# Kernel tuning notes

Hardware: AMD Instinct MI355X
Metric: run time of the kernel (lower is better)

## Reference

```python
import jax, jax.numpy as jnp
import numpy as np

N = 10000          # nodes
E = 160000         # edges (avg degree 16)
F = 240            # invariant features_dim
H_INV, D_INV = 4, 60    # invariant heads / head dim
H_EV, D_EV = 3, 80      # equivariant heads (= len(degrees)) / head dim
RBF = 32
DEGREES = [1, 2, 3]
REPEATS = np.array([2 * l + 1 for l in DEGREES])   # [3,5,7]
EV_DIM = int(REPEATS.sum())                        # 15
OFFS = np.concatenate([[0], np.cumsum(REPEATS)])   # [0,3,8,15]


def _kaiming_uniform(key, shape, fan_in):
    # torch kaiming_uniform_ with a=sqrt(5): bound = 1/sqrt(fan_in)
    b = 1.0 / np.sqrt(fan_in)
    return jax.random.uniform(key, shape, minval=-b, maxval=b, dtype=jnp.float32)


def setup_inputs() -> dict:
    key = jax.random.key(0)
    ks = jax.random.split(key, 16)
    return {
        "inv_features": jax.random.normal(ks[0], (N, F), dtype=jnp.float32),
        "ev_features": jax.random.normal(ks[1], (N, EV_DIM), dtype=jnp.float32),
        "rbf": jax.random.uniform(ks[2], (E, RBF), dtype=jnp.float32),
        "sh_vectors": jax.random.normal(ks[3], (E, EV_DIM), dtype=jnp.float32),
        "cutoffs": jax.random.uniform(ks[4], (E, 1), dtype=jnp.float32),
        "W_q_inv": _kaiming_uniform(ks[5], (H_INV, D_INV, D_INV), D_INV),
        "W_k_inv": _kaiming_uniform(ks[6], (H_INV, D_INV, D_INV), D_INV),
        "W_v_inv": _kaiming_uniform(ks[7], (H_INV, D_INV, D_INV), D_INV),
        "W_q_ev": _kaiming_uniform(ks[8], (H_EV, D_EV, D_EV), D_EV),
        "W_k_ev": _kaiming_uniform(ks[9], (H_EV, D_EV, D_EV), D_EV),
        "W_filt_inv": _kaiming_uniform(ks[10], (RBF + len(DEGREES), F), RBF + len(DEGREES)),
        "b_filt_inv": jnp.zeros((F,), dtype=jnp.float32),
        "W_filt_ev": _kaiming_uniform(ks[11], (RBF + len(DEGREES), F), RBF + len(DEGREES)),
        "b_filt_ev": jnp.zeros((F,), dtype=jnp.float32),
        "senders": jax.random.randint(ks[12], (E,), 0, N, dtype=jnp.int32),
        "receivers": jax.random.randint(ks[13], (E,), 0, N, dtype=jnp.int32),
    }


def reference(inv_features, ev_features, rbf, sh_vectors, cutoffs,
              W_q_inv, W_k_inv, W_v_inv, W_q_ev, W_k_ev,
              W_filt_inv, b_filt_inv, W_filt_ev, b_filt_ev,
              senders, receivers):
    n = inv_features.shape[0]
    # edge-wise equivariant differences [E, 15]
    ev_diff = ev_features[senders] - ev_features[receivers]
    # per-degree SO3 invariants: sum over m components of each degree -> [E, 3]
    invs = jnp.stack([(ev_diff[:, OFFS[i]:OFFS[i + 1]] ** 2).sum(-1)
                      for i in range(len(DEGREES))], axis=-1)
    f_in = jnp.concatenate([rbf, invs], axis=-1)           # [E, RBF+3]
    fw_inv = (f_in @ W_filt_inv + b_filt_inv).reshape(-1, H_INV, D_INV)
    fw_ev = (f_in @ W_filt_ev + b_filt_ev).reshape(-1, H_EV, D_EV)

    xi = inv_features.reshape(-1, H_INV, D_INV)
    xe = inv_features.reshape(-1, H_EV, D_EV)
    q_inv = jnp.einsum('hij,nhi->nhj', W_q_inv, xi)[receivers]
    k_inv = jnp.einsum('hij,nhi->nhj', W_k_inv, xi)[senders]
    v_inv = jnp.einsum('hij,nhi->nhj', W_v_inv, xi)[senders]
    q_ev = jnp.einsum('hij,nhi->nhj', W_q_ev, xe)[receivers]
    k_ev = jnp.einsum('hij,nhi->nhj', W_k_ev, xe)[senders]

    alpha_inv = (q_inv * (k_inv * fw_inv)).sum(-1, keepdims=True) / np.sqrt(D_INV)  # [E,H,1]
    alpha_ev = (q_ev * (k_ev * fw_ev)).sum(-1) / np.sqrt(D_EV)                      # [E,3]

    scaled_inv = cutoffs[:, None] * alpha_inv * v_inv       # [E,H,D]
    d_inv = jax.ops.segment_sum(scaled_inv, receivers, num_segments=n).reshape(n, -1)

    alpha_ev_r = jnp.repeat(alpha_ev, REPEATS, axis=-1, total_repeat_length=EV_DIM)  # [E,15]
    scaled_ev = cutoffs * alpha_ev_r * sh_vectors
    d_ev = jax.ops.segment_sum(scaled_ev, receivers, num_segments=n)
    return d_inv, d_ev
```

## Files before the change

kernel.cpp:

```cpp
#include <hip/hip_runtime.h>

#define PNPB 16
#define ABLK 128
#define EPT  4

__global__ __launch_bounds__(256) void proj_kernel(
    const float* __restrict__ x,
    const float* __restrict__ Wq, const float* __restrict__ Wk,
    const float* __restrict__ Wv,
    const float* __restrict__ Wqe, const float* __restrict__ Wke,
    float* __restrict__ q_inv, float* __restrict__ k_inv,
    float* __restrict__ v_inv,
    float* __restrict__ q_ev, float* __restrict__ k_ev, int N)
{
    __shared__ float xs[PNPB * 240];
    const int base_node = blockIdx.x * PNPB;
    for (int idx = threadIdx.x; idx < PNPB * 240; idx += 256) {
        int g = base_node * 240 + idx;
        xs[idx] = (g < N * 240) ? x[g] : 0.f;
    }
    __syncthreads();

    const int slot = threadIdx.x & 63;
    const int wg   = threadIdx.x >> 6;
    if (slot >= 60) return;

    const int hi  = slot / 15;
    const int jdi = slot * 4 - hi * 60;
    const int he  = slot / 20;
    const int jde = slot * 4 - he * 80;
    const int nl0 = wg * 4;

    float4 aq[4], ak[4], av[4], aqe[4], ake[4];
    #pragma unroll
    for (int n = 0; n < 4; ++n) {
        aq[n] = make_float4(0.f,0.f,0.f,0.f); ak[n] = aq[n]; av[n] = aq[n];
        aqe[n] = aq[n]; ake[n] = aq[n];
    }
    {
        const float* wq = Wq + hi * 3600 + jdi;
        const float* wk = Wk + hi * 3600 + jdi;
        const float* wv = Wv + hi * 3600 + jdi;
        const float* xb = &xs[nl0 * 240 + hi * 60];
        #pragma unroll 2
        for (int i = 0; i < 60; ++i) {
            float xv0 = xb[i], xv1 = xb[240 + i], xv2 = xb[480 + i], xv3 = xb[720 + i];
            float4 w;
            w = *(const float4*)&wq[i * 60];
            aq[0].x += xv0*w.x; aq[0].y += xv0*w.y; aq[0].z += xv0*w.z; aq[0].w += xv0*w.w;
            aq[1].x += xv1*w.x; aq[1].y += xv1*w.y; aq[1].z += xv1*w.z; aq[1].w += xv1*w.w;
            aq[2].x += xv2*w.x; aq[2].y += xv2*w.y; aq[2].z += xv2*w.z; aq[2].w += xv2*w.w;
            aq[3].x += xv3*w.x; aq[3].y += xv3*w.y; aq[3].z += xv3*w.z; aq[3].w += xv3*w.w;
            w = *(const float4*)&wk[i * 60];
            ak[0].x += xv0*w.x; ak[0].y += xv0*w.y; ak[0].z += xv0*w.z; ak[0].w += xv0*w.w;
            ak[1].x += xv1*w.x; ak[1].y += xv1*w.y; ak[1].z += xv1*w.z; ak[1].w += xv1*w.w;
            ak[2].x += xv2*w.x; ak[2].y += xv2*w.y; ak[2].z += xv2*w.z; ak[2].w += xv2*w.w;
            ak[3].x += xv3*w.x; ak[3].y += xv3*w.y; ak[3].z += xv3*w.z; ak[3].w += xv3*w.w;
            w = *(const float4*)&wv[i * 60];
            av[0].x += xv0*w.x; av[0].y += xv0*w.y; av[0].z += xv0*w.z; av[0].w += xv0*w.w;
            av[1].x += xv1*w.x; av[1].y += xv1*w.y; av[1].z += xv1*w.z; av[1].w += xv1*w.w;
            av[2].x += xv2*w.x; av[2].y += xv2*w.y; av[2].z += xv2*w.z; av[2].w += xv2*w.w;
            av[3].x += xv3*w.x; av[3].y += xv3*w.y; av[3].z += xv3*w.z; av[3].w += xv3*w.w;
        }
    }
    {
        const float* wq = Wqe + he * 6400 + jde;
        const float* wk = Wke + he * 6400 + jde;
        const float* xb = &xs[nl0 * 240 + he * 80];
        #pragma unroll 2
        for (int i = 0; i < 80; ++i) {
            float xv0 = xb[i], xv1 = xb[240 + i], xv2 = xb[480 + i], xv3 = xb[720 + i];
            float4 w;
            w = *(const float4*)&wq[i * 80];
            aqe[0].x += xv0*w.x; aqe[0].y += xv0*w.y; aqe[0].z += xv0*w.z; aqe[0].w += xv0*w.w;
            aqe[1].x += xv1*w.x; aqe[1].y += xv1*w.y; aqe[1].z += xv1*w.z; aqe[1].w += xv1*w.w;
            aqe[2].x += xv2*w.x; aqe[2].y += xv2*w.y; aqe[2].z += xv2*w.z; aqe[2].w += xv2*w.w;
            aqe[3].x += xv3*w.x; aqe[3].y += xv3*w.y; aqe[3].z += xv3*w.z; aqe[3].w += xv3*w.w;
            w = *(const float4*)&wk[i * 80];
            ake[0].x += xv0*w.x; ake[0].y += xv0*w.y; ake[0].z += xv0*w.z; ake[0].w += xv0*w.w;
            ake[1].x += xv1*w.x; ake[1].y += xv1*w.y; ake[1].z += xv1*w.z; ake[1].w += xv1*w.w;
            ake[2].x += xv2*w.x; ake[2].y += xv2*w.y; ake[2].z += xv2*w.z; ake[2].w += xv2*w.w;
            ake[3].x += xv3*w.x; ake[3].y += xv3*w.y; ake[3].z += xv3*w.z; ake[3].w += xv3*w.w;
        }
    }
    #pragma unroll
    for (int n = 0; n < 4; ++n) {
        const int node = base_node + nl0 + n;
        if (node >= N) break;
        const int ob = node * 240 + slot * 4;
        *(float4*)&q_inv[ob] = aq[n];
        *(float4*)&k_inv[ob] = ak[n];
        *(float4*)&v_inv[ob] = av[n];
        *(float4*)&q_ev[ob]  = aqe[n];
        *(float4*)&k_ev[ob]  = ake[n];
    }
}

__global__ __launch_bounds__(256) void hist_kernel(
    const int* __restrict__ rcv, int* __restrict__ counts, int E)
{
    int e = blockIdx.x * 256 + threadIdx.x;
    if (e < E) atomicAdd(&counts[rcv[e]], 1);
}

__global__ __launch_bounds__(1024) void scan_kernel(
    const int* __restrict__ counts, int* __restrict__ rowstart,
    int* __restrict__ cursor, int N)
{
    __shared__ int wsum[16];
    __shared__ int carry_s;
    if (threadIdx.x == 0) carry_s = 0;
    __syncthreads();
    const int lane = threadIdx.x & 63;
    const int w    = threadIdx.x >> 6;
    for (int base = 0; base < N; base += 1024) {
        const int i = base + threadIdx.x;
        int v = (i < N) ? counts[i] : 0;
        int x = v;
        #pragma unroll
        for (int off = 1; off < 64; off <<= 1) {
            int t = __shfl_up(x, off);
            if (lane >= off) x += t;
        }
        if (lane == 63) wsum[w] = x;
        __syncthreads();
        if (w == 0) {
            int s = (lane < 16) ? wsum[lane] : 0;
            #pragma unroll
            for (int off = 1; off < 16; off <<= 1) {
                int t = __shfl_up(s, off);
                if (lane >= off) s += t;
            }
            if (lane < 16) wsum[lane] = s;
        }
        __syncthreads();
        const int woff = (w == 0) ? 0 : wsum[w - 1];
        const int ex = carry_s + woff + x - v;
        if (i < N) { rowstart[i] = ex; cursor[i] = ex; }
        __syncthreads();
        if (threadIdx.x == 1023) carry_s += wsum[15];
    }
    __syncthreads();
    if (threadIdx.x == 0) rowstart[N] = carry_s;
}

__global__ __launch_bounds__(256) void scatter_kernel(
    const int* __restrict__ rcv, int* __restrict__ cursor,
    int* __restrict__ csr, int E)
{
    int e = blockIdx.x * 256 + threadIdx.x;
    if (e < E) {
        int pos = atomicAdd(&cursor[rcv[e]], 1);
        csr[pos] = e;
    }
}

__global__ __launch_bounds__(ABLK, 2) void alpha_kernel(
    const float* __restrict__ ev_f, const float* __restrict__ rbf,
    const float* __restrict__ cut,
    const float* __restrict__ Wfi,  const float* __restrict__ bfi,
    const float* __restrict__ Wfe,  const float* __restrict__ bfe,
    const int* __restrict__ snd,    const int* __restrict__ rcv,
    const int* __restrict__ csr,
    const float* __restrict__ q_inv, const float* __restrict__ k_inv,
    const float* __restrict__ q_ev,  const float* __restrict__ k_ev,
    float* __restrict__ alpha, int E)
{
    __shared__ float WI[35 * 240];
    __shared__ float WE[35 * 240];
    __shared__ float BI[240];
    __shared__ float BE[240];
    for (int idx = threadIdx.x; idx < 35 * 240; idx += ABLK) {
        WI[idx] = Wfi[idx];
        WE[idx] = Wfe[idx];
    }
    for (int idx = threadIdx.x; idx < 240; idx += ABLK) {
        BI[idx] = bfi[idx];
        BE[idx] = bfe[idx];
    }
    __syncthreads();

    const float s60 = 0.12909944487358056f;
    const float s80 = 0.11180339887498948f;

    const int base = blockIdx.x * (ABLK * EPT);

    int ii[EPT], sN[EPT], rN[EPT];
    float cc[EPT];
    float f[EPT][35];
    #pragma unroll
    for (int t = 0; t < EPT; ++t) {
        int i = base + t * ABLK + threadIdx.x;
        if (i >= E) i = E - 1;
        ii[t] = i;
        const int e = csr[i];
        sN[t] = snd[e]; rN[t] = rcv[e]; cc[t] = cut[e];
        const float4* rb = (const float4*)(rbf + (size_t)e * 32);
        #pragma unroll
        for (int k4 = 0; k4 < 8; ++k4) {
            float4 v = rb[k4];
            f[t][k4*4+0] = v.x; f[t][k4*4+1] = v.y;
            f[t][k4*4+2] = v.z; f[t][k4*4+3] = v.w;
        }
        const float* es = ev_f + (size_t)sN[t] * 15;
        const float* er = ev_f + (size_t)rN[t] * 15;
        float i0 = 0.f, i1 = 0.f, i2 = 0.f;
        #pragma unroll
        for (int q = 0; q < 3; ++q)  { float d = es[q] - er[q]; i0 += d * d; }
        #pragma unroll
        for (int q = 3; q < 8; ++q)  { float d = es[q] - er[q]; i1 += d * d; }
        #pragma unroll
        for (int q = 8; q < 15; ++q) { float d = es[q] - er[q]; i2 += d * d; }
        f[t][32] = i0; f[t][33] = i1; f[t][34] = i2;
    }

    float out[EPT][8];

    #pragma unroll
    for (int h = 0; h < 4; ++h) {
        float acc[EPT];
        #pragma unroll
        for (int t = 0; t < EPT; ++t) acc[t] = 0.f;
        #pragma unroll 1
        for (int j4 = 0; j4 < 15; ++j4) {
            const int j = h * 60 + j4 * 4;
            const float4 b4 = *(const float4*)&BI[j];
            float4 fw[EPT];
            #pragma unroll
            for (int t = 0; t < EPT; ++t) fw[t] = b4;
            #pragma unroll
            for (int k = 0; k < 35; ++k) {
                const float4 w = *(const float4*)&WI[k * 240 + j];
                #pragma unroll
                for (int t = 0; t < EPT; ++t) {
                    const float fv = f[t][k];
                    fw[t].x += fv * w.x; fw[t].y += fv * w.y;
                    fw[t].z += fv * w.z; fw[t].w += fv * w.w;
                }
            }
            #pragma unroll
            for (int t = 0; t < EPT; ++t) {
                const float4 q  = *(const float4*)(q_inv + (size_t)rN[t] * 240 + j);
                const float4 kk = *(const float4*)(k_inv + (size_t)sN[t] * 240 + j);
                acc[t] += q.x * kk.x * fw[t].x + q.y * kk.y * fw[t].y
                        + q.z * kk.z * fw[t].z + q.w * kk.w * fw[t].w;
            }
        }
        #pragma unroll
        for (int t = 0; t < EPT; ++t) out[t][h] = acc[t] * s60 * cc[t];
    }

    #pragma unroll
    for (int h = 0; h < 3; ++h) {
        float acc[EPT];
        #pragma unroll
        for (int t = 0; t < EPT; ++t) acc[t] = 0.f;
        #pragma unroll 1
        for (int j4 = 0; j4 < 20; ++j4) {
            const int j = h * 80 + j4 * 4;
            const float4 b4 = *(const float4*)&BE[j];
            float4 fw[EPT];
            #pragma unroll
            for (int t = 0; t < EPT; ++t) fw[t] = b4;
            #pragma unroll
            for (int k = 0; k < 35; ++k) {
                const float4 w = *(const float4*)&WE[k * 240 + j];
                #pragma unroll
                for (int t = 0; t < EPT; ++t) {
                    const float fv = f[t][k];
                    fw[t].x += fv * w.x; fw[t].y += fv * w.y;
                    fw[t].z += fv * w.z; fw[t].w += fv * w.w;
                }
            }
            #pragma unroll
            for (int t = 0; t < EPT; ++t) {
                const float4 q  = *(const float4*)(q_ev + (size_t)rN[t] * 240 + j);
                const float4 kk = *(const float4*)(k_ev + (size_t)sN[t] * 240 + j);
                acc[t] += q.x * kk.x * fw[t].x + q.y * kk.y * fw[t].y
                        + q.z * kk.z * fw[t].z + q.w * kk.w * fw[t].w;
            }
        }
        #pragma unroll
        for (int t = 0; t < EPT; ++t) out[t][4 + h] = acc[t] * s80 * cc[t];
    }

    #pragma unroll
    for (int t = 0; t < EPT; ++t) {
        out[t][7] = __int_as_float(sN[t]);
        float4* ap = (float4*)(alpha + (size_t)ii[t] * 8);
        ap[0] = make_float4(out[t][0], out[t][1], out[t][2], out[t][3]);
        ap[1] = make_float4(out[t][4], out[t][5], out[t][6], out[t][7]);
    }
}

__global__ __launch_bounds__(256) void gather_kernel(
    const int* __restrict__ rowstart, const int* __restrict__ csr,
    const float* __restrict__ alpha,
    const float* __restrict__ v_inv, const float* __restrict__ sh,
    float* __restrict__ dinv, float* __restrict__ dev)
{
    const int r = blockIdx.x;
    const int c = threadIdx.x;
    const int beg = rowstart[r], end = rowstart[r + 1];

    __shared__ float sal[64][8];
    __shared__ int   sed[64];

    float acc = 0.f;
    for (int chunk = beg; chunk < end; chunk += 64) {
        const int len = min(64, end - chunk);
        __syncthreads();
        if (c < len) {
            const float4* ap = (const float4*)(alpha + (size_t)(chunk + c) * 8);
            const float4 a0 = ap[0], a1 = ap[1];
            *(float4*)&sal[c][0] = a0;
            *(float4*)&sal[c][4] = a1;
            sed[c] = csr[chunk + c];
        }
        __syncthreads();
        if (c < 240) {
            const int h = c / 60;
            #pragma unroll 4
            for (int i = 0; i < len; ++i) {
                const int s = __float_as_int(sal[i][7]);
                acc += sal[i][h] * v_inv[(size_t)s * 240 + c];
            }
        } else if (c < 255) {
            const int i0 = c - 240;
            const int h = (i0 < 3) ? 4 : ((i0 < 8) ? 5 : 6);
            for (int i = 0; i < len; ++i)
                acc += sal[i][h] * sh[(size_t)sed[i] * 15 + i0];
        }
    }
    if (c < 240) dinv[(size_t)r * 240 + c] = acc;
    else if (c < 255) dev[(size_t)r * 15 + (c - 240)] = acc;
}

extern "C" void kernel_launch(void* const* d_in, const int* in_sizes, int n_in,
                              void* d_out, int out_size, void* d_ws, size_t ws_size,
                              hipStream_t stream) {
    const float* inv_f = (const float*)d_in[0];
    const float* ev_f  = (const float*)d_in[1];
    const float* rbf   = (const float*)d_in[2];
    const float* sh    = (const float*)d_in[3];
    const float* cut   = (const float*)d_in[4];
    const float* Wq    = (const float*)d_in[5];
    const float* Wk    = (const float*)d_in[6];
    const float* Wv    = (const float*)d_in[7];
    const float* Wqe   = (const float*)d_in[8];
    const float* Wke   = (const float*)d_in[9];
    const float* Wfi   = (const float*)d_in[10];
    const float* bfi   = (const float*)d_in[11];
    const float* Wfe   = (const float*)d_in[12];
    const float* bfe   = (const float*)d_in[13];
    const int*   snd   = (const int*)d_in[14];
    const int*   rcv   = (const int*)d_in[15];

    const int N = in_sizes[0] / 240;
    const int E = in_sizes[14];

    float* out  = (float*)d_out;
    float* dinv = out;
    float* dev  = out + (size_t)N * 240;

    float* ws = (float*)d_ws;
    const size_t Nf = (size_t)N * 240;
    float* q_inv = ws + 0 * Nf;
    float* k_inv = ws + 1 * Nf;
    float* v_inv = ws + 2 * Nf;
    float* q_ev  = ws + 3 * Nf;
    float* k_ev  = ws + 4 * Nf;
    float* alpha = ws + 5 * Nf;
    int*   ibase    = (int*)(alpha + (size_t)E * 8);
    int*   counts   = ibase;
    int*   rowstart = ibase + N;
    int*   cursor   = ibase + 2 * N + 1;
    int*   csr      = ibase + 3 * N + 1;

    hipMemsetAsync(counts, 0, (size_t)N * sizeof(int), stream);

    proj_kernel<<<(N + PNPB - 1) / PNPB, 256, 0, stream>>>(
        inv_f, Wq, Wk, Wv, Wqe, Wke, q_inv, k_inv, v_inv, q_ev, k_ev, N);

    const int eb = (E + 255) / 256;
    hist_kernel<<<eb, 256, 0, stream>>>(rcv, counts, E);
    scan_kernel<<<1, 1024, 0, stream>>>(counts, rowstart, cursor, N);
    scatter_kernel<<<eb, 256, 0, stream>>>(rcv, cursor, csr, E);

    const int ab = (E + ABLK * EPT - 1) / (ABLK * EPT);
    alpha_kernel<<<ab, ABLK, 0, stream>>>(
        ev_f, rbf, cut, Wfi, bfi, Wfe, bfe, snd, rcv, csr,
        q_inv, k_inv, q_ev, k_ev, alpha, E);

    gather_kernel<<<N, 256, 0, stream>>>(
        rowstart, csr, alpha, v_inv, sh, dinv, dev);
}
```

Baseline: 401.5 us.

## Split alpha kernel into wave-per-edge inv/ev kernels with register-resident filter weights

Replaces the single thread-per-edge alpha kernel, which kept both 35x240 filter matrices in shared memory, with two kernels in which each wave processes one edge at a time. A 16-lane group handles each head and keeps its slice of the filter weights in registers, then reduces the dot product with shuffles. The three edge invariants are precomputed by a separate small kernel. Alpha is now stored in original edge order, so the gather kernel loads it through the CSR index. The intent is to remove the shared-memory bandwidth bottleneck and make the q/k row reads coalesced, at the cost of high register pressure (140+ weight registers) and extra kernel launches.

Result: slower. 527.1 us (+31.3%).

```diff
diff --git a/kernel.cpp b/kernel.cpp
--- a/kernel.cpp
+++ b/kernel.cpp
@@ -1,8 +1,6 @@
 #include <hip/hip_runtime.h>
 
 #define PNPB 16
-#define ABLK 128
-#define EPT  4
 
 __global__ __launch_bounds__(256) void proj_kernel(
     const float* __restrict__ x,
@@ -155,141 +153,146 @@
     }
 }
 
-__global__ __launch_bounds__(ABLK, 2) void alpha_kernel(
-    const float* __restrict__ ev_f, const float* __restrict__ rbf,
+__global__ __launch_bounds__(256) void inv3_kernel(
+    const float* __restrict__ ev_f, const int* __restrict__ snd,
+    const int* __restrict__ rcv, float* __restrict__ inv3, int E)
+{
+    int e = blockIdx.x * 256 + threadIdx.x;
+    if (e >= E) return;
+    const float* es = ev_f + (size_t)snd[e] * 15;
+    const float* er = ev_f + (size_t)rcv[e] * 15;
+    float i0 = 0.f, i1 = 0.f, i2 = 0.f;
+    #pragma unroll
+    for (int q = 0; q < 3; ++q)  { float d = es[q] - er[q]; i0 = fmaf(d, d, i0); }
+    #pragma unroll
+    for (int q = 3; q < 8; ++q)  { float d = es[q] - er[q]; i1 = fmaf(d, d, i1); }
+    #pragma unroll
+    for (int q = 8; q < 15; ++q) { float d = es[q] - er[q]; i2 = fmaf(d, d, i2); }
+    *(float4*)(inv3 + (size_t)e * 4) = make_float4(i0, i1, i2, 0.f);
+}
+
+__global__ __launch_bounds__(128, 2) void alpha_inv_kernel(
+    const float* __restrict__ rbf, const float* __restrict__ inv3,
     const float* __restrict__ cut,
-    const float* __restrict__ Wfi,  const float* __restrict__ bfi,
-    const float* __restrict__ Wfe,  const float* __restrict__ bfe,
-    const int* __restrict__ snd,    const int* __restrict__ rcv,
-    const int* __restrict__ csr,
+    const float* __restrict__ Wfi, const float* __restrict__ bfi,
+    const int* __restrict__ snd, const int* __restrict__ rcv,
     const float* __restrict__ q_inv, const float* __restrict__ k_inv,
-    const float* __restrict__ q_ev,  const float* __restrict__ k_ev,
     float* __restrict__ alpha, int E)
 {
-    __shared__ float WI[35 * 240];
-    __shared__ float WE[35 * 240];
-    __shared__ float BI[240];
-    __shared__ float BE[240];
-    for (int idx = threadIdx.x; idx < 35 * 240; idx += ABLK) {
-        WI[idx] = Wfi[idx];
-        WE[idx] = Wfe[idx];
-    }
-    for (int idx = threadIdx.x; idx < 240; idx += ABLK) {
-        BI[idx] = bfi[idx];
-        BE[idx] = bfe[idx];
-    }
-    __syncthreads();
-
+    const int lane = threadIdx.x & 63;
+    const int wid  = __builtin_amdgcn_readfirstlane(threadIdx.x >> 6);
+    const int h = lane >> 4;
+    const int m = lane & 15;
+    const bool act = (m < 15);
+    const int j0 = h * 60 + (act ? m * 4 : 0);
+
+    float4 w[35];
+    #pragma unroll
+    for (int k = 0; k < 35; ++k)
+        w[k] = *(const float4*)(Wfi + k * 240 + j0);
+    const float4 b4 = *(const float4*)(bfi + j0);
     const float s60 = 0.12909944487358056f;
+
+    const int wbase = blockIdx.x * 128 + wid * 64;
+    #pragma unroll 2
+    for (int t = 0; t < 64; ++t) {
+        const int e = wbase + t;
+        if (e >= E) break;
+        const int s = snd[e];
+        const int r = rcv[e];
+        const float c = cut[e];
+        const float* rb = rbf + (size_t)e * 32;
+        const float* iv = inv3 + (size_t)e * 4;
+
+        float4 fw = b4;
+        #pragma unroll
+        for (int k = 0; k < 32; ++k) {
+            const float fk = rb[k];
+            fw.x = fmaf(fk, w[k].x, fw.x);
+            fw.y = fmaf(fk, w[k].y, fw.y);
+            fw.z = fmaf(fk, w[k].z, fw.z);
+            fw.w = fmaf(fk, w[k].w, fw.w);
+        }
+        #pragma unroll
+        for (int k = 32; k < 35; ++k) {
+            const float fk = iv[k - 32];
+            fw.x = fmaf(fk, w[k].x, fw.x);
+            fw.y = fmaf(fk, w[k].y, fw.y);
+            fw.z = fmaf(fk, w[k].z, fw.z);
+            fw.w = fmaf(fk, w[k].w, fw.w);
+        }
+        const float4 q  = *(const float4*)(q_inv + (size_t)r * 240 + j0);
+        const float4 kk = *(const float4*)(k_inv + (size_t)s * 240 + j0);
+        float d = act ? (q.x*kk.x*fw.x + q.y*kk.y*fw.y
+                       + q.z*kk.z*fw.z + q.w*kk.w*fw.w) : 0.f;
+        #pragma unroll
+        for (int off = 1; off < 16; off <<= 1) d += __shfl_xor(d, off, 16);
+        if (m == 0)    alpha[(size_t)e * 8 + h] = d * s60 * c;
+        if (lane == 0) alpha[(size_t)e * 8 + 7] = __int_as_float(s);
+    }
+}
+
+__global__ __launch_bounds__(128, 2) void alpha_ev_kernel(
+    const float* __restrict__ rbf, const float* __restrict__ inv3,
+    const float* __restrict__ cut,
+    const float* __restrict__ Wfe, const float* __restrict__ bfe,
+    const int* __restrict__ snd, const int* __restrict__ rcv,
+    const float* __restrict__ q_ev, const float* __restrict__ k_ev,
+    float* __restrict__ alpha, int E)
+{
+    const int lane = threadIdx.x & 63;
+    const int wid  = __builtin_amdgcn_readfirstlane(threadIdx.x >> 6);
+    const int h = lane >> 4;
+    const int m = lane & 15;
+    const bool act = (h < 3);
+    const int j0 = act ? (h * 80 + m * 5) : 0;
+
+    float w[35][5];
+    #pragma unroll
+    for (int k = 0; k < 35; ++k)
+        #pragma unroll
+        for (int cc = 0; cc < 5; ++cc)
+            w[k][cc] = Wfe[k * 240 + j0 + cc];
+    float b5[5];
+    #pragma unroll
+    for (int cc = 0; cc < 5; ++cc) b5[cc] = bfe[j0 + cc];
     const float s80 = 0.11180339887498948f;
 
-    const int base = blockIdx.x * (ABLK * EPT);
-
-    int ii[EPT], sN[EPT], rN[EPT];
-    float cc[EPT];
-    float f[EPT][35];
-    #pragma unroll
-    for (int t = 0; t < EPT; ++t) {
-        int i = base + t * ABLK + threadIdx.x;
-        if (i >= E) i = E - 1;
-        ii[t] = i;
-        const int e = csr[i];
-        sN[t] = snd[e]; rN[t] = rcv[e]; cc[t] = cut[e];
-        const float4* rb = (const float4*)(rbf + (size_t)e * 32);
-        #pragma unroll
-        for (int k4 = 0; k4 < 8; ++k4) {
-            float4 v = rb[k4];
-            f[t][k4*4+0] = v.x; f[t][k4*4+1] = v.y;
-            f[t][k4*4+2] = v.z; f[t][k4*4+3] = v.w;
-        }
-        const float* es = ev_f + (size_t)sN[t] * 15;
-        const float* er = ev_f + (size_t)rN[t] * 15;
-        float i0 = 0.f, i1 = 0.f, i2 = 0.f;
-        #pragma unroll
-        for (int q = 0; q < 3; ++q)  { float d = es[q] - er[q]; i0 += d * d; }
-        #pragma unroll
-        for (int q = 3; q < 8; ++q)  { float d = es[q] - er[q]; i1 += d * d; }
-        #pragma unroll
-        for (int q = 8; q < 15; ++q) { float d = es[q] - er[q]; i2 += d * d; }
-        f[t][32] = i0; f[t][33] = i1; f[t][34] = i2;
-    }
-
-    float out[EPT][8];
-
-    #pragma unroll
-    for (int h = 0; h < 4; ++h) {
-        float acc[EPT];
-        #pragma unroll
-        for (int t = 0; t < EPT; ++t) acc[t] = 0.f;
-        #pragma unroll 1
-        for (int j4 = 0; j4 < 15; ++j4) {
-            const int j = h * 60 + j4 * 4;
-            const float4 b4 = *(const float4*)&BI[j];
-            float4 fw[EPT];
+    const int wbase = blockIdx.x * 128 + wid * 64;
+    #pragma unroll 2
+    for (int t = 0; t < 64; ++t) {
+        const int e = wbase + t;
+        if (e >= E) break;
+        const int s = snd[e];
+        const int r = rcv[e];
+        const float c = cut[e];
+        const float* rb = rbf + (size_t)e * 32;
+        const float* iv = inv3 + (size_t)e * 4;
+
+        float fw[5];
+        #pragma unroll
+        for (int cc = 0; cc < 5; ++cc) fw[cc] = b5[cc];
+        #pragma unroll
+        for (int k = 0; k < 32; ++k) {
+            const float fk = rb[k];
             #pragma unroll
-            for (int t = 0; t < EPT; ++t) fw[t] = b4;
+            for (int cc = 0; cc < 5; ++cc) fw[cc] = fmaf(fk, w[k][cc], fw[cc]);
+        }
+        #pragma unroll
+        for (int k = 32; k < 35; ++k) {
+            const float fk = iv[k - 32];
             #pragma unroll
-            for (int k = 0; k < 35; ++k) {
-                const float4 w = *(const float4*)&WI[k * 240 + j];
-                #pragma unroll
-                for (int t = 0; t < EPT; ++t) {
-                    const float fv = f[t][k];
-                    fw[t].x += fv * w.x; fw[t].y += fv * w.y;
-                    fw[t].z += fv * w.z; fw[t].w += fv * w.w;
-                }
-            }
-            #pragma unroll
-            for (int t = 0; t < EPT; ++t) {
-                const float4 q  = *(const float4*)(q_inv + (size_t)rN[t] * 240 + j);
-                const float4 kk = *(const float4*)(k_inv + (size_t)sN[t] * 240 + j);
-                acc[t] += q.x * kk.x * fw[t].x + q.y * kk.y * fw[t].y
-                        + q.z * kk.z * fw[t].z + q.w * kk.w * fw[t].w;
-            }
-        }
-        #pragma unroll
-        for (int t = 0; t < EPT; ++t) out[t][h] = acc[t] * s60 * cc[t];
-    }
-
-    #pragma unroll
-    for (int h = 0; h < 3; ++h) {
-        float acc[EPT];
-        #pragma unroll
-        for (int t = 0; t < EPT; ++t) acc[t] = 0.f;
-        #pragma unroll 1
-        for (int j4 = 0; j4 < 20; ++j4) {
-            const int j = h * 80 + j4 * 4;
-            const float4 b4 = *(const float4*)&BE[j];
-            float4 fw[EPT];
-            #pragma unroll
-            for (int t = 0; t < EPT; ++t) fw[t] = b4;
-            #pragma unroll
-            for (int k = 0; k < 35; ++k) {
-                const float4 w = *(const float4*)&WE[k * 240 + j];
-                #pragma unroll
-                for (int t = 0; t < EPT; ++t) {
-                    const float fv = f[t][k];
-                    fw[t].x += fv * w.x; fw[t].y += fv * w.y;
-                    fw[t].z += fv * w.z; fw[t].w += fv * w.w;
-                }
-            }
-            #pragma unroll
-            for (int t = 0; t < EPT; ++t) {
-                const float4 q  = *(const float4*)(q_ev + (size_t)rN[t] * 240 + j);
-                const float4 kk = *(const float4*)(k_ev + (size_t)sN[t] * 240 + j);
-                acc[t] += q.x * kk.x * fw[t].x + q.y * kk.y * fw[t].y
-                        + q.z * kk.z * fw[t].z + q.w * kk.w * fw[t].w;
-            }
-        }
-        #pragma unroll
-        for (int t = 0; t < EPT; ++t) out[t][4 + h] = acc[t] * s80 * cc[t];
-    }
-
-    #pragma unroll
-    for (int t = 0; t < EPT; ++t) {
-        out[t][7] = __int_as_float(sN[t]);
-        float4* ap = (float4*)(alpha + (size_t)ii[t] * 8);
-        ap[0] = make_float4(out[t][0], out[t][1], out[t][2], out[t][3]);
-        ap[1] = make_float4(out[t][4], out[t][5], out[t][6], out[t][7]);
+            for (int cc = 0; cc < 5; ++cc) fw[cc] = fmaf(fk, w[k][cc], fw[cc]);
+        }
+        const float* qp  = q_ev + (size_t)r * 240 + j0;
+        const float* kp  = k_ev + (size_t)s * 240 + j0;
+        float d = 0.f;
+        #pragma unroll
+        for (int cc = 0; cc < 5; ++cc) d = fmaf(qp[cc] * kp[cc], fw[cc], d);
+        if (!act) d = 0.f;
+        #pragma unroll
+        for (int off = 1; off < 16; off <<= 1) d += __shfl_xor(d, off, 16);
+        if (m == 0 && act) alpha[(size_t)e * 8 + 4 + h] = d * s80 * c;
     }
 }
 
@@ -311,11 +314,12 @@
         const int len = min(64, end - chunk);
         __syncthreads();
         if (c < len) {
-            const float4* ap = (const float4*)(alpha + (size_t)(chunk + c) * 8);
+            const int ed = csr[chunk + c];
+            sed[c] = ed;
+            const float4* ap = (const float4*)(alpha + (size_t)ed * 8);
             const float4 a0 = ap[0], a1 = ap[1];
             *(float4*)&sal[c][0] = a0;
             *(float4*)&sal[c][4] = a1;
-            sed[c] = csr[chunk + c];
         }
         __syncthreads();
         if (c < 240) {
@@ -371,7 +375,8 @@
     float* q_ev  = ws + 3 * Nf;
     float* k_ev  = ws + 4 * Nf;
     float* alpha = ws + 5 * Nf;
-    int*   ibase    = (int*)(alpha + (size_t)E * 8);
+    float* inv3  = alpha + (size_t)E * 8;
+    int*   ibase    = (int*)(inv3 + (size_t)E * 4);
     int*   counts   = ibase;
     int*   rowstart = ibase + N;
     int*   cursor   = ibase + 2 * N + 1;
@@ -379,18 +384,21 @@
 
     hipMemsetAsync(counts, 0, (size_t)N * sizeof(int), stream);
 
-    proj_kernel<<<(N + PNPB - 1) / PNPB, 256, 0, stream>>>(
-        inv_f, Wq, Wk, Wv, Wqe, Wke, q_inv, k_inv, v_inv, q_ev, k_ev, N);
-
     const int eb = (E + 255) / 256;
     hist_kernel<<<eb, 256, 0, stream>>>(rcv, counts, E);
     scan_kernel<<<1, 1024, 0, stream>>>(counts, rowstart, cursor, N);
     scatter_kernel<<<eb, 256, 0, stream>>>(rcv, cursor, csr, E);
 
-    const int ab = (E + ABLK * EPT - 1) / (ABLK * EPT);
-    alpha_kernel<<<ab, ABLK, 0, stream>>>(
-        ev_f, rbf, cut, Wfi, bfi, Wfe, bfe, snd, rcv, csr,
-        q_inv, k_inv, q_ev, k_ev, alpha, E);
+    proj_kernel<<<(N + PNPB - 1) / PNPB, 256, 0, stream>>>(
+        inv_f, Wq, Wk, Wv, Wqe, Wke, q_inv, k_inv, v_inv, q_ev, k_ev, N);
+
+    inv3_kernel<<<eb, 256, 0, stream>>>(ev_f, snd, rcv, inv3, E);
+
+    const int ab = (E + 127) / 128;
+    alpha_inv_kernel<<<ab, 128, 0, stream>>>(
+        rbf, inv3, cut, Wfi, bfi, snd, rcv, q_inv, k_inv, alpha, E);
+    alpha_ev_kernel<<<ab, 128, 0, stream>>>(
+        rbf, inv3, cut, Wfe, bfe, snd, rcv, q_ev, k_ev, alpha, E);
 
     gather_kernel<<<N, 256, 0, stream>>>(
         rowstart, csr, alpha, v_inv, sh, dinv, dev);
```
